# Performance work log

Hardware: AMD Instinct MI355X
Metric: run time of the kernel (lower is better)

The kernel has to match this reference:

```python
import jax, jax.numpy as jnp
import numpy as np

N = 100000      # physical-network nodes
E = 3200000     # directed edges (avg degree 32)
DIN = 128       # input_dim
DH = 128        # embedding_dim
DOUT = 128      # output_dim
NUM_GRAPHS = 1


def setup_inputs() -> dict:
    key = jax.random.key(0)
    ks = jax.random.split(key, 8)
    s = 0.05
    x = jax.random.normal(ks[0], (N, DIN), dtype=jnp.float32)
    edge_index = jax.random.randint(ks[1], (2, E), 0, N, dtype=jnp.int64)
    W1 = jax.random.normal(ks[2], (DIN, DH), dtype=jnp.float32) * s
    b1 = jnp.zeros((DH,), dtype=jnp.float32)
    W2 = jax.random.normal(ks[3], (DH, DH), dtype=jnp.float32) * s
    b2 = jnp.zeros((DH,), dtype=jnp.float32)
    W3 = jax.random.normal(ks[4], (DH, DOUT), dtype=jnp.float32) * s
    b3 = jnp.zeros((DOUT,), dtype=jnp.float32)
    return {"x": x, "edge_index": edge_index,
            "W1": W1, "b1": b1, "W2": W2, "b2": b2, "W3": W3, "b3": b3}


def _gcn_norm(edge_index, n_nodes):
    # PyG GCNConv default: add self-loops, symmetric D^{-1/2} (A+I) D^{-1/2} norm.
    loops = jnp.arange(n_nodes, dtype=edge_index.dtype)
    src = jnp.concatenate([edge_index[0], loops])   # [E+N]
    dst = jnp.concatenate([edge_index[1], loops])   # [E+N]
    deg = jax.ops.segment_sum(jnp.ones_like(dst, dtype=jnp.float32), dst,
                              num_segments=n_nodes)
    dinv = jax.lax.rsqrt(deg)  # deg >= 1 because of self-loops
    norm = dinv[src] * dinv[dst]                    # [E+N]
    return src, dst, norm


def _gcn_conv(h, W, b, src, dst, norm, n_nodes):
    h = h @ W                                       # [N, dout] linear first (PyG order)
    msg = h[src] * norm[:, None]                    # gather + edge scaling
    agg = jax.ops.segment_sum(msg, dst, num_segments=n_nodes)  # scatter-add
    return agg + b


def reference(x, edge_index, W1, b1, W2, b2, W3, b3):
    src, dst, norm = _gcn_norm(edge_index, N)
    h = jax.nn.relu(_gcn_conv(x, W1, b1, src, dst, norm, N))
    # dropout is identity in eval mode
    h = jax.nn.relu(_gcn_conv(h, W2, b2, src, dst, norm, N))
    h = _gcn_conv(h, W3, b3, src, dst, norm, N)
    return h.reshape(NUM_GRAPHS, N // NUM_GRAPHS, -1)
```

## Files before the change

### kernel.cpp

```cpp
#include <hip/hip_runtime.h>
#include <cstddef>
#include <cstdint>

#define NN 100000
#define NE 3200000
#define D  128
#define NB 782
#define BSH 7
#define NPB 512
#define CHUNK 6250
#define BCAP 4608

typedef short v8s __attribute__((ext_vector_type(8)));
typedef float v4f __attribute__((ext_vector_type(4)));


__device__ __forceinline__ unsigned short f2bf(float f) {
  uint32_t u = __float_as_uint(f);
  uint32_t r = u + 0x7fff + ((u >> 16) & 1);
  return (unsigned short)(r >> 16);
}
__device__ __forceinline__ float bf_lo(uint32_t v) {
  return __uint_as_float(v << 16);
}
__device__ __forceinline__ float bf_hi(uint32_t v) {
  return __uint_as_float(v & 0xffff0000u);
}


__global__ __launch_bounds__(256) void kb_part2(const int* __restrict__ src,
                                                const int* __restrict__ dst,
                                                int* __restrict__ gcur,
                                                uint32_t* __restrict__ ebuf) {
  __shared__ int h[NB];
  __shared__ int cur[NB];
  for (int i = threadIdx.x; i < NB; i += 256) h[i] = 0;
  __syncthreads();
  int lo = blockIdx.x * CHUNK, hi = lo + CHUNK;
  if (hi > NE) hi = NE;
  for (int e = lo + threadIdx.x; e < hi; e += 256)
    atomicAdd(&h[dst[e] >> BSH], 1);
  __syncthreads();
  for (int i = threadIdx.x; i < NB; i += 256)
    cur[i] = h[i] ? atomicAdd(&gcur[i], h[i]) : 0;
  __syncthreads();
  for (int e = lo + threadIdx.x; e < hi; e += 256) {
    int s = src[e], d = dst[e];
    int b = d >> BSH;
    int p = atomicAdd(&cur[b], 1);
    if (p < BCAP)
      ebuf[(size_t)b * BCAP + p] = ((uint32_t)s << BSH) | (uint32_t)(d & 127);
  }
}

__global__ __launch_bounds__(256) void kb_build(const uint32_t* __restrict__ ebuf,
                                                const int* __restrict__ gcur,
                                                int* __restrict__ row_off,
                                                int* __restrict__ row_end,
                                                float* __restrict__ dinv,
                                                int* __restrict__ col) {
  int b = blockIdx.x;
  __shared__ int h[128];
  __shared__ int s[128];
  __shared__ int cur[128];
  if (threadIdx.x < 128) h[threadIdx.x] = 0;
  __syncthreads();
  const uint32_t* eb = ebuf + (size_t)b * BCAP;
  int cnt = gcur[b];
  for (int e = threadIdx.x; e < cnt; e += 256)
    atomicAdd(&h[eb[e] & 127], 1);
  __syncthreads();
  int v = (threadIdx.x < 128) ? h[threadIdx.x] : 0;
  if (threadIdx.x < 128) s[threadIdx.x] = v;
  __syncthreads();
  for (int d = 1; d < 128; d <<= 1) {
    int t = (threadIdx.x < 128 && threadIdx.x >= d) ? s[threadIdx.x - d] : 0;
    __syncthreads();
    if (threadIdx.x < 128) s[threadIdx.x] += t;
    __syncthreads();
  }
  if (threadIdx.x < 128) {
    int ro = b * BCAP + s[threadIdx.x] - v;
    cur[threadIdx.x] = ro;
    int node = b * 128 + threadIdx.x;
    if (node < NN) {
      row_off[node] = ro;
      row_end[node] = ro + v;
      dinv[node] = rsqrtf((float)(v + 1));
    }
  }
  __syncthreads();
  for (int e = threadIdx.x; e < cnt; e += 256) {
    uint32_t p = eb[e];
    int pos = atomicAdd(&cur[p & 127], 1);
    col[pos] = (int)(p >> BSH);
  }
}


__global__ void k_wt3z(const float* __restrict__ W1, const float* __restrict__ W2,
                       const float* __restrict__ W3, unsigned short* __restrict__ wt,
                       int* __restrict__ gcur) {
  int idx = blockIdx.x * 256 + threadIdx.x;
  if (idx < NB) gcur[idx] = 0;
  if (idx >= 3 * 16384) return;
  int m = idx >> 14, rem = idx & 16383;
  int k = rem >> 7, c = rem & 127;
  const float* W = (m == 0) ? W1 : (m == 1) ? W2 : W3;
  wt[m * 16384 + c * 128 + k] = f2bf(W[rem]);
}


__global__ __launch_bounds__(256) void k_gemm2(const float* __restrict__ A,
                                               const unsigned short* __restrict__ wt,
                                               const float* __restrict__ dinv,
                                               unsigned short* __restrict__ C) {
  const int wave = threadIdx.x >> 6;
  const int lane = threadIdx.x & 63;
  const int row0 = blockIdx.x * 256 + wave * 64;
  const int rl = lane & 15;
  const int kg = lane >> 4;

  v4f acc[4][8];
#pragma unroll
  for (int t = 0; t < 4; ++t)
#pragma unroll
    for (int ct = 0; ct < 8; ++ct) acc[t][ct] = (v4f){0.f, 0.f, 0.f, 0.f};

  union U { uint4 u; v8s v; unsigned short us[8]; };

#pragma unroll
  for (int ks = 0; ks < 4; ++ks) {
    U a[4];
#pragma unroll
    for (int t = 0; t < 4; ++t) {
      int r = row0 + t * 16 + rl;
      if (r >= NN) r = NN - 1;
      const float* ap = A + (size_t)r * D + ks * 32 + kg * 8;
      float4 l4 = *(const float4*)ap;
      float4 h4 = *(const float4*)(ap + 4);
      a[t].us[0] = f2bf(l4.x); a[t].us[1] = f2bf(l4.y);
      a[t].us[2] = f2bf(l4.z); a[t].us[3] = f2bf(l4.w);
      a[t].us[4] = f2bf(h4.x); a[t].us[5] = f2bf(h4.y);
      a[t].us[6] = f2bf(h4.z); a[t].us[7] = f2bf(h4.w);
    }
#pragma unroll
    for (int ct = 0; ct < 8; ++ct) {
      U b;
      b.u = *(const uint4*)(wt + (size_t)(ct * 16 + rl) * 128 + ks * 32 + kg * 8);
#pragma unroll
      for (int t = 0; t < 4; ++t)
        acc[t][ct] =
            __builtin_amdgcn_mfma_f32_16x16x32_bf16(a[t].v, b.v, acc[t][ct], 0, 0, 0);
    }
  }

#pragma unroll
  for (int t = 0; t < 4; ++t) {
#pragma unroll
    for (int i = 0; i < 4; ++i) {
      int row = row0 + t * 16 + kg * 4 + i;
      if (row < NN) {
        float dv = dinv[row];
#pragma unroll
        for (int ct = 0; ct < 8; ++ct)
          C[(size_t)row * D + ct * 16 + rl] = f2bf(dv * acc[t][ct][i]);
      }
    }
  }
}


#define AGG8(e0, q0, q1)                                     \
  {                                                          \
    int s0 = col[e0], s1 = col[e0 + 1], s2 = col[e0 + 2],    \
        s3 = col[e0 + 3], s4 = col[e0 + 4], s5 = col[e0 + 5],\
        s6 = col[e0 + 6], s7 = col[e0 + 7];                  \
    uint32_t v0 = tu[(size_t)s0 * 64 + lane];                \
    uint32_t v1 = tu[(size_t)s1 * 64 + lane];                \
    uint32_t v2 = tu[(size_t)s2 * 64 + lane];                \
    uint32_t v3 = tu[(size_t)s3 * 64 + lane];                \
    uint32_t v4 = tu[(size_t)s4 * 64 + lane];                \
    uint32_t v5 = tu[(size_t)s5 * 64 + lane];                \
    uint32_t v6 = tu[(size_t)s6 * 64 + lane];                \
    uint32_t v7 = tu[(size_t)s7 * 64 + lane];                \
    q0 += bf_lo(v0); q1 += bf_hi(v0);                        \
    q0 += bf_lo(v1); q1 += bf_hi(v1);                        \
    q0 += bf_lo(v2); q1 += bf_hi(v2);                        \
    q0 += bf_lo(v3); q1 += bf_hi(v3);                        \
    q0 += bf_lo(v4); q1 += bf_hi(v4);                        \
    q0 += bf_lo(v5); q1 += bf_hi(v5);                        \
    q0 += bf_lo(v6); q1 += bf_hi(v6);                        \
    q0 += bf_lo(v7); q1 += bf_hi(v7);                        \
  }

#define GATHER_BODY()                                                        \
  uint32_t svA = tu[(size_t)gA * 64 + lane];                                 \
  uint32_t svB = tu[(size_t)gB * 64 + lane];                                 \
  float a0 = bf_lo(svA), a1 = bf_hi(svA);                                    \
  float b0 = bf_lo(svB), b1 = bf_hi(svB);                                    \
  int eA = row_off[gA], endA = row_end[gA];                                  \
  int eB = row_off[gB], endB = row_end[gB];                                  \
  while (eA + 8 <= endA && eB + 8 <= endB) {                                 \
    int sA0 = col[eA],     sA1 = col[eA + 1], sA2 = col[eA + 2],             \
        sA3 = col[eA + 3], sA4 = col[eA + 4], sA5 = col[eA + 5],             \
        sA6 = col[eA + 6], sA7 = col[eA + 7];                                \
    int sB0 = col[eB],     sB1 = col[eB + 1], sB2 = col[eB + 2],             \
        sB3 = col[eB + 3], sB4 = col[eB + 4], sB5 = col[eB + 5],             \
        sB6 = col[eB + 6], sB7 = col[eB + 7];                                \
    uint32_t vA0 = tu[(size_t)sA0 * 64 + lane];                              \
    uint32_t vA1 = tu[(size_t)sA1 * 64 + lane];                              \
    uint32_t vA2 = tu[(size_t)sA2 * 64 + lane];                              \
    uint32_t vA3 = tu[(size_t)sA3 * 64 + lane];                              \
    uint32_t vA4 = tu[(size_t)sA4 * 64 + lane];                              \
    uint32_t vA5 = tu[(size_t)sA5 * 64 + lane];                              \
    uint32_t vA6 = tu[(size_t)sA6 * 64 + lane];                              \
    uint32_t vA7 = tu[(size_t)sA7 * 64 + lane];                              \
    uint32_t vB0 = tu[(size_t)sB0 * 64 + lane];                              \
    uint32_t vB1 = tu[(size_t)sB1 * 64 + lane];                              \
    uint32_t vB2 = tu[(size_t)sB2 * 64 + lane];                              \
    uint32_t vB3 = tu[(size_t)sB3 * 64 + lane];                              \
    uint32_t vB4 = tu[(size_t)sB4 * 64 + lane];                              \
    uint32_t vB5 = tu[(size_t)sB5 * 64 + lane];                              \
    uint32_t vB6 = tu[(size_t)sB6 * 64 + lane];                              \
    uint32_t vB7 = tu[(size_t)sB7 * 64 + lane];                              \
    a0 += bf_lo(vA0); a1 += bf_hi(vA0);                                      \
    a0 += bf_lo(vA1); a1 += bf_hi(vA1);                                      \
    a0 += bf_lo(vA2); a1 += bf_hi(vA2);                                      \
    a0 += bf_lo(vA3); a1 += bf_hi(vA3);                                      \
    a0 += bf_lo(vA4); a1 += bf_hi(vA4);                                      \
    a0 += bf_lo(vA5); a1 += bf_hi(vA5);                                      \
    a0 += bf_lo(vA6); a1 += bf_hi(vA6);                                      \
    a0 += bf_lo(vA7); a1 += bf_hi(vA7);                                      \
    b0 += bf_lo(vB0); b1 += bf_hi(vB0);                                      \
    b0 += bf_lo(vB1); b1 += bf_hi(vB1);                                      \
    b0 += bf_lo(vB2); b1 += bf_hi(vB2);                                      \
    b0 += bf_lo(vB3); b1 += bf_hi(vB3);                                      \
    b0 += bf_lo(vB4); b1 += bf_hi(vB4);                                      \
    b0 += bf_lo(vB5); b1 += bf_hi(vB5);                                      \
    b0 += bf_lo(vB6); b1 += bf_hi(vB6);                                      \
    b0 += bf_lo(vB7); b1 += bf_hi(vB7);                                      \
    eA += 8; eB += 8;                                                        \
  }                                                                          \
  for (; eA + 8 <= endA; eA += 8) AGG8(eA, a0, a1);                          \
  for (; eA < endA; ++eA) {                                                  \
    uint32_t v = tu[(size_t)col[eA] * 64 + lane];                            \
    a0 += bf_lo(v); a1 += bf_hi(v);                                          \
  }                                                                          \
  for (; eB + 8 <= endB; eB += 8) AGG8(eB, b0, b1);                          \
  for (; eB < endB; ++eB) {                                                  \
    uint32_t v = tu[(size_t)col[eB] * 64 + lane];                            \
    b0 += bf_lo(v); b1 += bf_hi(v);                                          \
  }


__global__ __launch_bounds__(256) void k_aggf(
    const uint32_t* __restrict__ tu, const int* __restrict__ row_off,
    const int* __restrict__ row_end, const int* __restrict__ col,
    const float* __restrict__ dinv, const float* __restrict__ bias,
    const unsigned short* __restrict__ wt, unsigned short* __restrict__ t_out) {
  const int wave = threadIdx.x >> 6;
  const int lane = threadIdx.x & 63;
  const int base = blockIdx.x * 64 + wave * 16;

  __shared__ uint32_t lds[4][16 * 64];
  uint32_t* lw = lds[wave];

  const int c = lane * 2;
  const float bl = bias[c], bh = bias[c + 1];

#pragma unroll 1
  for (int p = 0; p < 8; ++p) {
    int gA = base + 2 * p;
    int gB = gA + 1;
    if (gA >= NN) gA = NN - 1;
    if (gB >= NN) gB = NN - 1;
    const float diA = dinv[gA], diB = dinv[gB];

    GATHER_BODY();

    uint32_t packA = (uint32_t)f2bf(fmaxf(diA * a0 + bl, 0.f)) |
                     ((uint32_t)f2bf(fmaxf(diA * a1 + bh, 0.f)) << 16);
    uint32_t packB = (uint32_t)f2bf(fmaxf(diB * b0 + bl, 0.f)) |
                     ((uint32_t)f2bf(fmaxf(diB * b1 + bh, 0.f)) << 16);
    const int rA = 2 * p, rB = rA + 1;
    lw[rA * 64 + (lane ^ ((rA & 7) << 2))] = packA;
    lw[rB * 64 + (lane ^ ((rB & 7) << 2))] = packB;
  }

  const int rl = lane & 15;
  const int kg = lane >> 4;
  union U { uint4 u; v8s v; };

  float di4[4];
#pragma unroll
  for (int i = 0; i < 4; ++i) {
    int node = base + kg * 4 + i;
    di4[i] = dinv[node < NN ? node : NN - 1];
  }

#pragma unroll
  for (int ct = 0; ct < 8; ++ct) {
    v4f acc = (v4f){0.f, 0.f, 0.f, 0.f};
#pragma unroll
    for (int ks = 0; ks < 4; ++ks) {
      U a, b;
      a.u = *(const uint4*)&lw[rl * 64 + ((ks * 16 + kg * 4) ^ ((rl & 7) << 2))];
      b.u = *(const uint4*)(wt + (size_t)(ct * 16 + rl) * 128 + ks * 32 + kg * 8);
      acc = __builtin_amdgcn_mfma_f32_16x16x32_bf16(a.v, b.v, acc, 0, 0, 0);
    }
#pragma unroll
    for (int i = 0; i < 4; ++i) {
      int node = base + kg * 4 + i;
      if (node < NN)
        t_out[(size_t)node * D + ct * 16 + rl] = f2bf(di4[i] * acc[i]);
    }
  }
}


__global__ __launch_bounds__(256) void k_agg2(
    const uint32_t* __restrict__ tu, const int* __restrict__ row_off,
    const int* __restrict__ row_end, const int* __restrict__ col,
    const float* __restrict__ dinv, const float* __restrict__ bias,
    float* __restrict__ outf) {
  const int wave = threadIdx.x >> 6;
  const int lane = threadIdx.x & 63;
  const int gA = blockIdx.x * 8 + wave * 2;
  const int gB = gA + 1;

  const float diA = dinv[gA], diB = dinv[gB];

  GATHER_BODY();

  int c = lane * 2;
  float rA0 = diA * a0 + bias[c];
  float rA1 = diA * a1 + bias[c + 1];
  float rB0 = diB * b0 + bias[c];
  float rB1 = diB * b1 + bias[c + 1];
  *(float2*)(outf + (size_t)gA * D + c) = make_float2(rA0, rA1);
  *(float2*)(outf + (size_t)gB * D + c) = make_float2(rB0, rB1);
}


extern "C" void kernel_launch(void* const* d_in, const int* in_sizes, int n_in,
                              void* d_out, int out_size, void* d_ws, size_t ws_size,
                              hipStream_t stream) {
  const float* x  = (const float*)d_in[0];
  const int*   ei = (const int*)d_in[1];
  const float* W1 = (const float*)d_in[2];
  const float* b1 = (const float*)d_in[3];
  const float* W2 = (const float*)d_in[4];
  const float* b2 = (const float*)d_in[5];
  const float* W3 = (const float*)d_in[6];
  const float* b3 = (const float*)d_in[7];
  float* out = (float*)d_out;

  char* base = (char*)d_ws;
  size_t o = 0;
  auto take = [&](size_t bytes) {
    void* p = base + o;
    o += (bytes + 255) & ~(size_t)255;
    return p;
  };
  int*   row_off = (int*)take((size_t)NN * 4);
  int*   row_end = (int*)take((size_t)NN * 4);
  float* dinv    = (float*)take((size_t)NN * 4);
  int*   gcur    = (int*)take((size_t)NB * 4);
  unsigned short* wt = (unsigned short*)take(3 * 16384 * 2);
  void* region1 = take((size_t)NN * D * 2);
  int*  col     = (int*)take((size_t)NB * BCAP * 4);
  unsigned short* t0 = (unsigned short*)take((size_t)NN * D * 2);

  uint32_t* ebuf = (uint32_t*)region1;
  unsigned short* t1 = (unsigned short*)region1;

  const int* src = ei;
  const int* dst = ei + NE;

  k_wt3z  <<<192, 256, 0, stream>>>(W1, W2, W3, wt, gcur);
  kb_part2<<<NPB, 256, 0, stream>>>(src, dst, gcur, ebuf);
  kb_build<<<NB, 256, 0, stream>>>(ebuf, gcur, row_off, row_end, dinv, col);

  const int gB = (NN + 255) / 256;
  const int fB = (NN + 63) / 64;
  const int aB = NN / 8;

  k_gemm2<<<gB, 256, 0, stream>>>(x, wt, dinv, t0);
  k_aggf<<<fB, 256, 0, stream>>>((const uint32_t*)t0, row_off, row_end, col, dinv,
                                 b1, wt + 16384, t1);
  k_aggf<<<fB, 256, 0, stream>>>((const uint32_t*)t1, row_off, row_end, col, dinv,
                                 b2, wt + 32768, t0);
  k_agg2<<<aB, 256, 0, stream>>>((const uint32_t*)t0, row_off, row_end, col, dinv,
                                 b3, out);
}
```

Baseline: 482.5 us.

## Pad CSR rows to multiples of eight and vector-load column indices

The CSR build now rounds each node's neighbor count up to a multiple of 8. Padding slots point to a dummy node NN whose feature row is zeroed in the extra slot of each feature buffer. This lets the aggregation drop its scalar tail loops and fetch column indices as two 128-bit nontemporal loads per 8 edges instead of eight scalar loads. The cost is extra gathers of the zero row, a larger per-bucket capacity and a slightly larger workspace.

```diff
diff --git a/kernel.cpp b/kernel.cpp
--- a/kernel.cpp
+++ b/kernel.cpp
@@ -9,10 +9,13 @@
 #define BSH 7
 #define NPB 512
 #define CHUNK 6250
-#define BCAP 4608
+#define BCAP 4992
 
 typedef short v8s __attribute__((ext_vector_type(8)));
 typedef float v4f __attribute__((ext_vector_type(4)));
+typedef int   v4i __attribute__((ext_vector_type(4)));
+
+#define NTL4(p) __builtin_nontemporal_load((const v4i*)(p))
 
 
 __device__ __forceinline__ unsigned short f2bf(float f) {
@@ -67,11 +70,13 @@
   __syncthreads();
   const uint32_t* eb = ebuf + (size_t)b * BCAP;
   int cnt = gcur[b];
+  if (cnt > BCAP) cnt = BCAP;
   for (int e = threadIdx.x; e < cnt; e += 256)
     atomicAdd(&h[eb[e] & 127], 1);
   __syncthreads();
   int v = (threadIdx.x < 128) ? h[threadIdx.x] : 0;
-  if (threadIdx.x < 128) s[threadIdx.x] = v;
+  int vp = (v + 7) & ~7;
+  if (threadIdx.x < 128) s[threadIdx.x] = vp;
   __syncthreads();
   for (int d = 1; d < 128; d <<= 1) {
     int t = (threadIdx.x < 128 && threadIdx.x >= d) ? s[threadIdx.x - d] : 0;
@@ -80,29 +85,38 @@
     __syncthreads();
   }
   if (threadIdx.x < 128) {
-    int ro = b * BCAP + s[threadIdx.x] - v;
+    int ro = b * BCAP + s[threadIdx.x] - vp;
     cur[threadIdx.x] = ro;
     int node = b * 128 + threadIdx.x;
     if (node < NN) {
       row_off[node] = ro;
-      row_end[node] = ro + v;
+      row_end[node] = ro + vp;
       dinv[node] = rsqrtf((float)(v + 1));
+      for (int j = v; j < vp; ++j) {
+        int pos = ro + j;
+        if (pos < NB * BCAP) col[pos] = NN;
+      }
     }
   }
   __syncthreads();
   for (int e = threadIdx.x; e < cnt; e += 256) {
     uint32_t p = eb[e];
     int pos = atomicAdd(&cur[p & 127], 1);
-    col[pos] = (int)(p >> BSH);
+    if (pos < NB * BCAP) col[pos] = (int)(p >> BSH);
   }
 }
 
 
 __global__ void k_wt3z(const float* __restrict__ W1, const float* __restrict__ W2,
                        const float* __restrict__ W3, unsigned short* __restrict__ wt,
-                       int* __restrict__ gcur) {
+                       int* __restrict__ gcur, unsigned short* __restrict__ t0,
+                       unsigned short* __restrict__ t1) {
   int idx = blockIdx.x * 256 + threadIdx.x;
   if (idx < NB) gcur[idx] = 0;
+  if (idx < 16)
+    ((uint4*)(t0 + (size_t)NN * D))[idx] = make_uint4(0, 0, 0, 0);
+  else if (idx < 32)
+    ((uint4*)(t1 + (size_t)NN * D))[idx - 16] = make_uint4(0, 0, 0, 0);
   if (idx >= 3 * 16384) return;
   int m = idx >> 14, rem = idx & 16383;
   int k = rem >> 7, c = rem & 127;
@@ -173,17 +187,16 @@
 
 #define AGG8(e0, q0, q1)                                     \
   {                                                          \
-    int s0 = col[e0], s1 = col[e0 + 1], s2 = col[e0 + 2],    \
-        s3 = col[e0 + 3], s4 = col[e0 + 4], s5 = col[e0 + 5],\
-        s6 = col[e0 + 6], s7 = col[e0 + 7];                  \
-    uint32_t v0 = tu[(size_t)s0 * 64 + lane];                \
-    uint32_t v1 = tu[(size_t)s1 * 64 + lane];                \
-    uint32_t v2 = tu[(size_t)s2 * 64 + lane];                \
-    uint32_t v3 = tu[(size_t)s3 * 64 + lane];                \
-    uint32_t v4 = tu[(size_t)s4 * 64 + lane];                \
-    uint32_t v5 = tu[(size_t)s5 * 64 + lane];                \
-    uint32_t v6 = tu[(size_t)s6 * 64 + lane];                \
-    uint32_t v7 = tu[(size_t)s7 * 64 + lane];                \
+    v4i c0 = NTL4(col + (e0));                               \
+    v4i c1 = NTL4(col + (e0) + 4);                           \
+    uint32_t v0 = tu[(size_t)c0[0] * 64 + lane];             \
+    uint32_t v1 = tu[(size_t)c0[1] * 64 + lane];             \
+    uint32_t v2 = tu[(size_t)c0[2] * 64 + lane];             \
+    uint32_t v3 = tu[(size_t)c0[3] * 64 + lane];             \
+    uint32_t v4 = tu[(size_t)c1[0] * 64 + lane];             \
+    uint32_t v5 = tu[(size_t)c1[1] * 64 + lane];             \
+    uint32_t v6 = tu[(size_t)c1[2] * 64 + lane];             \
+    uint32_t v7 = tu[(size_t)c1[3] * 64 + lane];             \
     q0 += bf_lo(v0); q1 += bf_hi(v0);                        \
     q0 += bf_lo(v1); q1 += bf_hi(v1);                        \
     q0 += bf_lo(v2); q1 += bf_hi(v2);                        \
@@ -202,28 +215,24 @@
   int eA = row_off[gA], endA = row_end[gA];                                  \
   int eB = row_off[gB], endB = row_end[gB];                                  \
   while (eA + 8 <= endA && eB + 8 <= endB) {                                 \
-    int sA0 = col[eA],     sA1 = col[eA + 1], sA2 = col[eA + 2],             \
-        sA3 = col[eA + 3], sA4 = col[eA + 4], sA5 = col[eA + 5],             \
-        sA6 = col[eA + 6], sA7 = col[eA + 7];                                \
-    int sB0 = col[eB],     sB1 = col[eB + 1], sB2 = col[eB + 2],             \
-        sB3 = col[eB + 3], sB4 = col[eB + 4], sB5 = col[eB + 5],             \
-        sB6 = col[eB + 6], sB7 = col[eB + 7];                                \
-    uint32_t vA0 = tu[(size_t)sA0 * 64 + lane];                              \
-    uint32_t vA1 = tu[(size_t)sA1 * 64 + lane];                              \
-    uint32_t vA2 = tu[(size_t)sA2 * 64 + lane];                              \
-    uint32_t vA3 = tu[(size_t)sA3 * 64 + lane];                              \
-    uint32_t vA4 = tu[(size_t)sA4 * 64 + lane];                              \
-    uint32_t vA5 = tu[(size_t)sA5 * 64 + lane];                              \
-    uint32_t vA6 = tu[(size_t)sA6 * 64 + lane];                              \
-    uint32_t vA7 = tu[(size_t)sA7 * 64 + lane];                              \
-    uint32_t vB0 = tu[(size_t)sB0 * 64 + lane];                              \
-    uint32_t vB1 = tu[(size_t)sB1 * 64 + lane];                              \
-    uint32_t vB2 = tu[(size_t)sB2 * 64 + lane];                              \
-    uint32_t vB3 = tu[(size_t)sB3 * 64 + lane];                              \
-    uint32_t vB4 = tu[(size_t)sB4 * 64 + lane];                              \
-    uint32_t vB5 = tu[(size_t)sB5 * 64 + lane];                              \
-    uint32_t vB6 = tu[(size_t)sB6 * 64 + lane];                              \
-    uint32_t vB7 = tu[(size_t)sB7 * 64 + lane];                              \
+    v4i cA0 = NTL4(col + eA); v4i cA1 = NTL4(col + eA + 4);                  \
+    v4i cB0 = NTL4(col + eB); v4i cB1 = NTL4(col + eB + 4);                  \
+    uint32_t vA0 = tu[(size_t)cA0[0] * 64 + lane];                           \
+    uint32_t vA1 = tu[(size_t)cA0[1] * 64 + lane];                           \
+    uint32_t vA2 = tu[(size_t)cA0[2] * 64 + lane];                           \
+    uint32_t vA3 = tu[(size_t)cA0[3] * 64 + lane];                           \
+    uint32_t vA4 = tu[(size_t)cA1[0] * 64 + lane];                           \
+    uint32_t vA5 = tu[(size_t)cA1[1] * 64 + lane];                           \
+    uint32_t vA6 = tu[(size_t)cA1[2] * 64 + lane];                           \
+    uint32_t vA7 = tu[(size_t)cA1[3] * 64 + lane];                           \
+    uint32_t vB0 = tu[(size_t)cB0[0] * 64 + lane];                           \
+    uint32_t vB1 = tu[(size_t)cB0[1] * 64 + lane];                           \
+    uint32_t vB2 = tu[(size_t)cB0[2] * 64 + lane];                           \
+    uint32_t vB3 = tu[(size_t)cB0[3] * 64 + lane];                           \
+    uint32_t vB4 = tu[(size_t)cB1[0] * 64 + lane];                           \
+    uint32_t vB5 = tu[(size_t)cB1[1] * 64 + lane];                           \
+    uint32_t vB6 = tu[(size_t)cB1[2] * 64 + lane];                           \
+    uint32_t vB7 = tu[(size_t)cB1[3] * 64 + lane];                           \
     a0 += bf_lo(vA0); a1 += bf_hi(vA0);                                      \
     a0 += bf_lo(vA1); a1 += bf_hi(vA1);                                      \
     a0 += bf_lo(vA2); a1 += bf_hi(vA2);                                      \
@@ -243,15 +252,7 @@
     eA += 8; eB += 8;                                                        \
   }                                                                          \
   for (; eA + 8 <= endA; eA += 8) AGG8(eA, a0, a1);                          \
-  for (; eA < endA; ++eA) {                                                  \
-    uint32_t v = tu[(size_t)col[eA] * 64 + lane];                            \
-    a0 += bf_lo(v); a1 += bf_hi(v);                                          \
-  }                                                                          \
-  for (; eB + 8 <= endB; eB += 8) AGG8(eB, b0, b1);                          \
-  for (; eB < endB; ++eB) {                                                  \
-    uint32_t v = tu[(size_t)col[eB] * 64 + lane];                            \
-    b0 += bf_lo(v); b1 += bf_hi(v);                                          \
-  }
+  for (; eB + 8 <= endB; eB += 8) AGG8(eB, b0, b1);
 
 
 __global__ __launch_bounds__(256) void k_aggf(
@@ -368,9 +369,9 @@
   float* dinv    = (float*)take((size_t)NN * 4);
   int*   gcur    = (int*)take((size_t)NB * 4);
   unsigned short* wt = (unsigned short*)take(3 * 16384 * 2);
-  void* region1 = take((size_t)NN * D * 2);
+  void* region1 = take((size_t)(NN + 1) * D * 2);
   int*  col     = (int*)take((size_t)NB * BCAP * 4);
-  unsigned short* t0 = (unsigned short*)take((size_t)NN * D * 2);
+  unsigned short* t0 = (unsigned short*)take((size_t)(NN + 1) * D * 2);
 
   uint32_t* ebuf = (uint32_t*)region1;
   unsigned short* t1 = (unsigned short*)region1;
@@ -378,7 +379,7 @@
   const int* src = ei;
   const int* dst = ei + NE;
 
-  k_wt3z  <<<192, 256, 0, stream>>>(W1, W2, W3, wt, gcur);
+  k_wt3z  <<<192, 256, 0, stream>>>(W1, W2, W3, wt, gcur, t0, t1);
   kb_part2<<<NPB, 256, 0, stream>>>(src, dst, gcur, ebuf);
   kb_build<<<NB, 256, 0, stream>>>(ebuf, gcur, row_off, row_end, dinv, col);
 
```

Result: slower. 504.0 us (+4.5%).
